# Optimization experiments

Hardware: AMD Instinct MI355X
Metric: run time of the kernel (lower is better)

Reference implementation:

```python
import jax, jax.numpy as jnp
import numpy as np

B, N, E = 2, 2048, 1024
H, D = 16, 64


def setup_inputs() -> dict:
    key = jax.random.key(0)
    k1, k2, k3 = jax.random.split(key, 3)
    x = jax.random.normal(k1, (B, N, E), dtype=jnp.float32)
    Wqkv = jax.random.normal(k2, (3 * H * D, E), dtype=jnp.float32) * 0.02
    bqkv = jnp.zeros((3 * H * D,), dtype=jnp.float32)
    Wout = jax.random.normal(k3, (E, H * D), dtype=jnp.float32) * 0.02
    bout = jnp.zeros((E,), dtype=jnp.float32)
    return {"x": x, "Wqkv": Wqkv, "bqkv": bqkv, "Wout": Wout, "bout": bout}


def reference(x, Wqkv, bqkv, Wout, bout):
    b, n, _ = x.shape
    scale = D ** (-0.5)
    # qkv projection: [b, n, 3*h*d], interpreted as (h, d, qkv) per einops pattern
    qkv = (x @ Wqkv.T + bqkv).reshape(b, n, H, D, 3)
    q = jnp.transpose(qkv[..., 0], (0, 2, 1, 3))  # [b, h, n, d]
    k = jnp.transpose(qkv[..., 1], (0, 2, 1, 3))
    v = jnp.transpose(qkv[..., 2], (0, 2, 1, 3))
    att = jnp.einsum('bhid,bhjd->bhij', q, k) * scale  # [b, h, n, n]
    causal = jnp.tril(jnp.ones((n, n), dtype=bool))
    att = jnp.where(causal, att, -jnp.inf)
    att = jax.nn.softmax(att, axis=-1)
    out = jnp.einsum('bhij,bhjd->bhid', att, v)  # [b, h, n, d]
    out = jnp.transpose(out, (0, 2, 1, 3)).reshape(b, n, H * D)
    return out @ Wout.T + bout
```

## Files before the change

### kernel.cpp

```cpp
#include <hip/hip_runtime.h>
#include <hip/hip_bf16.h>

#define B_ 2
#define N_ 2048
#define E_ 1024
#define H_ 16
#define D_ 64
#define M_ 4096
#define HD_ 1024
#define NT_ 3072

using f32x4  = __attribute__((ext_vector_type(4))) float;
using f32x16 = __attribute__((ext_vector_type(16))) float;
using bf16x8 = __attribute__((ext_vector_type(8))) short;

static __device__ __forceinline__ unsigned short f2bf(float f) {
  union { float f; unsigned u; } v; v.f = f;
  unsigned r = v.u + 0x7FFF + ((v.u >> 16) & 1);
  return (unsigned short)(r >> 16);
}
static __device__ __forceinline__ float bf2f(short s) {
  union { unsigned u; float f; } v; v.u = ((unsigned)(unsigned short)s) << 16; return v.f;
}

static __device__ __forceinline__ void gld16(const void* g, void* l) {
  __builtin_amdgcn_global_load_lds(
      (const __attribute__((address_space(1))) unsigned int*)g,
      (__attribute__((address_space(3))) unsigned int*)l, 16, 0, 0);
}

static __device__ __forceinline__ unsigned cvtpk(float lo, float hi) {
  unsigned r;
  asm("v_cvt_pk_bf16_f32 %0, %1, %2" : "=v"(r) : "v"(lo), "v"(hi));
  return r;
}
static __device__ __forceinline__ void pl32swap(unsigned& a, unsigned& b) {
  asm("v_permlane32_swap_b32 %0, %1" : "+v"(a), "+v"(b));
}


__global__ void k_cvt_x(const float* __restrict__ x, unsigned short* __restrict__ xb) {
  int t = blockIdx.x * 256 + threadIdx.x;
  float4 v = reinterpret_cast<const float4*>(x)[t];
  ushort4 o;
  o.x = f2bf(v.x); o.y = f2bf(v.y); o.z = f2bf(v.z); o.w = f2bf(v.w);
  reinterpret_cast<ushort4*>(xb)[t] = o;
}

__global__ void k_cvt_wqkv(const float* __restrict__ w, const float* __restrict__ bsrc,
                           unsigned short* __restrict__ wb, float* __restrict__ br) {
  int t = blockIdx.x * 256 + threadIdx.x;
  int r = t >> 8;
  int c = (t & 255) * 4;
  int kind = r >> 10, hd = r & 1023;
  int h = hd >> 6, d = hd & 63;
  int rin = h * 192 + d * 3 + kind;
  float s = (kind == 0) ? 0.125f * 1.4426950408889634f : 1.0f;
  float4 v = *reinterpret_cast<const float4*>(w + (size_t)rin * E_ + c);
  ushort4 o;
  o.x = f2bf(v.x * s); o.y = f2bf(v.y * s); o.z = f2bf(v.z * s); o.w = f2bf(v.w * s);
  *reinterpret_cast<ushort4*>(wb + (size_t)r * E_ + c) = o;
  if (c == 0) br[r] = bsrc[rin] * s;
}

__global__ void k_cvt_wout(const float* __restrict__ w, unsigned short* __restrict__ wb) {
  int t = blockIdx.x * 256 + threadIdx.x;
  int r = t >> 8;
  int c = (t & 255) * 4;
  float4 v = *reinterpret_cast<const float4*>(w + (size_t)r * HD_ + c);
  ushort4 o;
  o.x = f2bf(v.x); o.y = f2bf(v.y); o.z = f2bf(v.z); o.w = f2bf(v.w);
  *reinterpret_cast<ushort4*>(wb + (size_t)r * HD_ + c) = o;
}

template <int EPI>
__global__ __launch_bounds__(256, 2) void k_gemm(
    const unsigned short* __restrict__ A,
    const unsigned short* __restrict__ W,
    const float* __restrict__ bias,
    unsigned short* __restrict__ Qo, unsigned short* __restrict__ Ko,
    unsigned short* __restrict__ Vo, float* __restrict__ Fo,
    int M, int Nt, int K)
{
  __shared__ unsigned short As[128 * 32];
  __shared__ unsigned short Bs[128 * 32];
  const int t = threadIdx.x;
  const int w = t >> 6, l = t & 63, lg = l >> 4, lr = l & 15;
  const int wm = w >> 1, wn = w & 1;
  const int row0 = blockIdx.x * 128, col0 = blockIdx.y * 128;

  f32x4 acc[4][4] = {};

  for (int k0 = 0; k0 < K; k0 += 32) {
#pragma unroll
    for (int c = 0; c < 2; ++c) {
      int ci = w * 2 + c;
      int eo = ci * 512 + l * 8;
      int rr = eo >> 5, kk = eo & 31;
      gld16(A + (size_t)(row0 + rr) * K + k0 + kk, (unsigned short*)As + ci * 512);
      gld16(W + (size_t)(col0 + rr) * K + k0 + kk, (unsigned short*)Bs + ci * 512);
    }
    __syncthreads();
    bf16x8 af[4], bf[4];
#pragma unroll
    for (int m = 0; m < 4; ++m)
      af[m] = *reinterpret_cast<const bf16x8*>(&As[(wm * 64 + m * 16 + lr) * 32 + lg * 8]);
#pragma unroll
    for (int n = 0; n < 4; ++n)
      bf[n] = *reinterpret_cast<const bf16x8*>(&Bs[(wn * 64 + n * 16 + lr) * 32 + lg * 8]);
#pragma unroll
    for (int m = 0; m < 4; ++m)
#pragma unroll
      for (int n = 0; n < 4; ++n)
        acc[m][n] = __builtin_amdgcn_mfma_f32_16x16x32_bf16(af[m], bf[n], acc[m][n], 0, 0, 0);
    __syncthreads();
  }

#pragma unroll
  for (int m = 0; m < 4; ++m) {
#pragma unroll
    for (int n = 0; n < 4; ++n) {
      int col = col0 + wn * 64 + n * 16 + lr;
      float bb = bias[col];
#pragma unroll
      for (int rr = 0; rr < 4; ++rr) {
        int ro = row0 + wm * 64 + m * 16 + lg * 4 + rr;
        float val = acc[m][n][rr] + bb;
        if (EPI == 0) {
          int kind = col >> 10, hd = col & 1023, h = hd >> 6, d = hd & 63;
          int bi = ro >> 11, ni = ro & 2047;
          unsigned short bv = f2bf(val);
          size_t bh = (size_t)(bi * H_ + h);
          if (kind == 0)      Qo[(bh * N_ + ni) * D_ + d] = bv;
          else if (kind == 1) Ko[(bh * N_ + ni) * D_ + d] = bv;
          else                Vo[bh * (size_t)(D_ * N_) + (size_t)d * N_ + ni] = bv;
        } else {
          Fo[(size_t)ro * HD_ + col] = val;
        }
      }
    }
  }
}

__global__ __launch_bounds__(256, 3) void k_attn(
    const unsigned short* __restrict__ Q,
    const unsigned short* __restrict__ Kg,
    const unsigned short* __restrict__ Vg,
    unsigned short* __restrict__ O,
    unsigned short* __restrict__ Pp,
    float* __restrict__ Pml)
{
  static const int u_qt[24] = {15,15,14,13,12,11,10, 9,   8, 7,14, 6,13, 5,12, 4,   8, 0, 9, 1,10, 2,11, 3};
  static const int u_t0[24] = { 0,16, 0, 0, 0, 0, 0, 0,   0, 0,16, 0,16, 0,16, 0,  16, 0,16, 0,16, 0,16, 0};
  static const int u_ps[24] = {14,15,12,10, 8, 6, 4, 2,   0,-1,13,-1,11,-1, 9,-1,   1,-1, 3,-1, 5,-1, 7,-1};

  __shared__ unsigned short Ks[2][64 * 64];
  __shared__ unsigned short Vs[2][64 * 64];

  const int t = threadIdx.x;
  const int w = t >> 6, l = t & 63;
  const int lq = l & 31;
  const int hi = l >> 5;
  const int bh = blockIdx.x & 31;
  const int u  = blockIdx.x >> 5;
  const int qt = u_qt[u], t0 = u_t0[u], ps = u_ps[u];
  const int q0 = qt * 128;
  const int r0w = q0 + w * 32;
  const int rtop = r0w + 31;
  const bool splitc0 = (ps >= 0) && (t0 == 0);
  const int tendW = splitc0 ? 16 : ((rtop >> 6) + 1);
  const int tendB = splitc0 ? 16 : (((q0 + 127) >> 6) + 1);

  const unsigned short* Qb = Q  + (size_t)bh * (N_ * D_);
  const unsigned short* Kb = Kg + (size_t)bh * (N_ * D_);
  const unsigned short* Vb = Vg + (size_t)bh * (N_ * D_);

  const int pr  = l >> 3;
  const int pswz = ((l & 7) ^ pr) * 8;
  const unsigned short* KsrcB = Kb + pr * D_ + pswz;
  const unsigned short* VsrcB = Vb + pr * N_ + pswz;

  bf16x8 qf[4];
#pragma unroll
  for (int ks = 0; ks < 4; ++ks)
    qf[ks] = *reinterpret_cast<const bf16x8*>(
        Qb + (size_t)(r0w + lq) * D_ + ks * 16 + hi * 8);

  f32x16 oacc[2] = {};
  float lrun = 0.f;

  {
    const int kv0 = t0 * 64;
#pragma unroll
    for (int c = 0; c < 2; ++c) {
      int cb = w * 2 + c;
      gld16(KsrcB + kv0 * D_ + cb * 512, (unsigned short*)&Ks[0][0] + cb * 512);
      gld16(VsrcB + kv0 + cb * 8 * N_,   (unsigned short*)&Vs[0][0] + cb * 512);
    }
  }
  __syncthreads();
  int buf = 0;

  for (int kt = t0; kt < tendB; ++kt) {
    const int kv0 = kt * 64;

    if (kt + 1 < tendB) {
      const int kv1 = kv0 + 64;
#pragma unroll
      for (int c = 0; c < 2; ++c) {
        int cb = w * 2 + c;
        gld16(KsrcB + kv1 * D_ + cb * 512, (unsigned short*)&Ks[buf ^ 1][0] + cb * 512);
        gld16(VsrcB + kv1 + cb * 8 * N_,   (unsigned short*)&Vs[buf ^ 1][0] + cb * 512);
      }
    }

    if (kt < tendW) {
      bf16x8 kf[2][4], vf[2][4];
#pragma unroll
      for (int ct = 0; ct < 2; ++ct)
#pragma unroll
        for (int ks = 0; ks < 4; ++ks) {
          int row = ct * 32 + lq;
          kf[ct][ks] = *reinterpret_cast<const bf16x8*>(
              &Ks[buf][row * 64 + (((ks * 2 + hi) ^ (lq & 7)) * 8)]);
        }
#pragma unroll
      for (int dt = 0; dt < 2; ++dt)
#pragma unroll
        for (int j = 0; j < 4; ++j) {
          int row = dt * 32 + lq;
          vf[dt][j] = *reinterpret_cast<const bf16x8*>(
              &Vs[buf][row * 64 + (((j * 2 + hi) ^ (lq & 7)) * 8)]);
        }

      f32x16 sct[2];
      __builtin_amdgcn_s_setprio(1);
#pragma unroll
      for (int ct = 0; ct < 2; ++ct) {
        f32x16 z = {};
#pragma unroll
        for (int ks = 0; ks < 4; ++ks)
          z = __builtin_amdgcn_mfma_f32_32x32x16_bf16(kf[ct][ks], qf[ks], z, 0, 0, 0);
        sct[ct] = z;
      }
      __builtin_amdgcn_s_setprio(0);

      if (kv0 + 63 > r0w) {
        int qrow = r0w + lq;
#pragma unroll
        for (int ct = 0; ct < 2; ++ct)
#pragma unroll
          for (int r = 0; r < 16; ++r) {
            int kv = kv0 + ct * 32 + (r & 3) + 8 * (r >> 2) + 4 * hi;
            if (kv > qrow) sct[ct][r] = -1e30f;
          }
      }

      float s16[16];
#pragma unroll
      for (int r = 0; r < 16; ++r) {
        float p0 = exp2f(sct[0][r]);
        float p1 = exp2f(sct[1][r]);
        sct[0][r] = p0; sct[1][r] = p1;
        s16[r] = p0 + p1;
      }
#pragma unroll
      for (int st = 8; st >= 1; st >>= 1)
#pragma unroll
        for (int r = 0; r < 8; ++r)
          if (r < st) s16[r] += s16[r + st];
      lrun += s16[0] + __shfl_xor(s16[0], 32);

      bf16x8 paf[4];
#pragma unroll
      for (int ct = 0; ct < 2; ++ct) {
        unsigned u0 = cvtpk(sct[ct][0],  sct[ct][1]);
        unsigned u1 = cvtpk(sct[ct][2],  sct[ct][3]);
        unsigned u2 = cvtpk(sct[ct][4],  sct[ct][5]);
        unsigned u3 = cvtpk(sct[ct][6],  sct[ct][7]);
        unsigned u4 = cvtpk(sct[ct][8],  sct[ct][9]);
        unsigned u5 = cvtpk(sct[ct][10], sct[ct][11]);
        unsigned u6 = cvtpk(sct[ct][12], sct[ct][13]);
        unsigned u7 = cvtpk(sct[ct][14], sct[ct][15]);
        pl32swap(u0, u2); pl32swap(u1, u3);
        pl32swap(u4, u6); pl32swap(u5, u7);
        union { unsigned uu[4]; bf16x8 v; } c0, c1;
        c0.uu[0] = u0; c0.uu[1] = u1; c0.uu[2] = u2; c0.uu[3] = u3;
        c1.uu[0] = u4; c1.uu[1] = u5; c1.uu[2] = u6; c1.uu[3] = u7;
        paf[ct * 2]     = c0.v;
        paf[ct * 2 + 1] = c1.v;
      }

      __builtin_amdgcn_s_setprio(1);
#pragma unroll
      for (int dt = 0; dt < 2; ++dt)
#pragma unroll
        for (int j = 0; j < 4; ++j)
          oacc[dt] = __builtin_amdgcn_mfma_f32_32x32x16_bf16(paf[j], vf[dt][j], oacc[dt], 0, 0, 0);
      __builtin_amdgcn_s_setprio(0);
    }

    __syncthreads();
    buf ^= 1;
  }

  int bi = bh >> 4, h = bh & 15;
  if (ps < 0) {
    float inv = 1.0f / lrun;
    float iv[16];
#pragma unroll
    for (int r = 0; r < 16; ++r)
      iv[r] = __shfl(inv, (r & 3) + 8 * (r >> 2) + 4 * hi);
#pragma unroll
    for (int dt = 0; dt < 2; ++dt)
#pragma unroll
      for (int r = 0; r < 16; ++r) {
        int qr = r0w + (r & 3) + 8 * (r >> 2) + 4 * hi;
        int d = dt * 32 + lq;
        O[((size_t)(bi * N_ + qr) * H_ + h) * D_ + d] = f2bf(oacc[dt][r] * iv[r]);
      }
  } else {
    unsigned short* pb = Pp + (size_t)(bh * 16 + ps) * (128 * 64);
    float* mb = Pml + (size_t)(bh * 16 + ps) * 128;
#pragma unroll
    for (int dt = 0; dt < 2; ++dt)
#pragma unroll
      for (int r = 0; r < 16; ++r) {
        int rloc = w * 32 + (r & 3) + 8 * (r >> 2) + 4 * hi;
        pb[rloc * 64 + dt * 32 + lq] = f2bf(oacc[dt][r]);
      }
    if (l < 32) {
      int rloc = w * 32 + l;
      mb[rloc] = lrun;
    }
  }
}

__global__ void k_merge(const unsigned short* __restrict__ Pp,
                        const float* __restrict__ Pml,
                        unsigned short* __restrict__ O) {
  int t = blockIdx.x * 256 + threadIdx.x;
  int dseg = t & 7;
  int rloc = (t >> 3) & 127;
  int qt8 = (t >> 10) & 7;
  int bh  = t >> 13;
  size_t b0 = (size_t)(bh * 16 + qt8 * 2) * 128 + rloc;
  size_t b1 = b0 + 128;
  bf16x8 o0 = *reinterpret_cast<const bf16x8*>(Pp + b0 * 64 + dseg * 8);
  bf16x8 o1 = *reinterpret_cast<const bf16x8*>(Pp + b1 * 64 + dseg * 8);
  float l0 = Pml[b0], l1 = Pml[b1];
  float inv = 1.0f / (l0 + l1);
  int n = (qt8 + 8) * 128 + rloc;
  int bi = bh >> 4, h = bh & 15;
  unsigned short* op = O + ((size_t)(bi * N_ + n) * H_ + h) * D_ + dseg * 8;
  bf16x8 res;
#pragma unroll
  for (int j = 0; j < 8; ++j)
    res[j] = (short)f2bf((bf2f(o0[j]) + bf2f(o1[j])) * inv);
  *reinterpret_cast<bf16x8*>(op) = res;
}


extern "C" void kernel_launch(void* const* d_in, const int* in_sizes, int n_in,
                              void* d_out, int out_size, void* d_ws, size_t ws_size,
                              hipStream_t stream) {
  const float* x    = (const float*)d_in[0];
  const float* Wqkv = (const float*)d_in[1];
  const float* bqkv = (const float*)d_in[2];
  const float* Wout = (const float*)d_in[3];
  const float* bout = (const float*)d_in[4];
  float* out = (float*)d_out;

  char* ws = (char*)d_ws;
  unsigned short* xb  = (unsigned short*)ws; ws += (size_t)M_ * E_ * 2;
  unsigned short* wqb = (unsigned short*)ws; ws += (size_t)NT_ * E_ * 2;
  float*          bqr = (float*)ws;          ws += 16384;
  unsigned short* wob = (unsigned short*)ws; ws += (size_t)E_ * HD_ * 2;
  unsigned short* Qb  = (unsigned short*)ws; ws += (size_t)M_ * D_ * H_ * 2;
  unsigned short* Kb  = (unsigned short*)ws; ws += (size_t)M_ * D_ * H_ * 2;
  unsigned short* Vb  = (unsigned short*)ws; ws += (size_t)M_ * D_ * H_ * 2;
  unsigned short* ao  = (unsigned short*)ws; ws += (size_t)M_ * HD_ * 2;

  unsigned short* Pp  = xb;
  float*          Pml = (float*)wqb;

  k_cvt_x<<<(M_ * E_) / 4 / 256, 256, 0, stream>>>(x, xb);
  k_cvt_wqkv<<<NT_, 256, 0, stream>>>(Wqkv, bqkv, wqb, bqr);
  k_cvt_wout<<<E_, 256, 0, stream>>>(Wout, wob);

  k_gemm<0><<<dim3(M_ / 128, NT_ / 128), 256, 0, stream>>>(
      xb, wqb, bqr, Qb, Kb, Vb, nullptr, M_, NT_, E_);

  k_attn<<<768, 256, 0, stream>>>(Qb, Kb, Vb, ao, Pp, Pml);
  k_merge<<<1024, 256, 0, stream>>>(Pp, Pml, ao);

  k_gemm<1><<<dim3(M_ / 128, HD_ / 128), 256, 0, stream>>>(
      ao, wob, bout, nullptr, nullptr, nullptr, out, M_, HD_, E_);
}
```

Measured before the change: 119.0 us.

## Triple-buffer GEMM and attention loads with vmcnt waits, swizzled LDS, smaller out-proj tile

Both the GEMM and attention kernels move from a double-buffered __syncthreads loop to a three-stage ring of global_load_lds prefetches. Each stage is gated by an explicit s_waitcnt vmcnt count and a raw s_barrier, so two tiles are in flight while the current one is consumed. The GEMM LDS tiles gain an XOR swizzle to reduce bank conflicts on fragment reads. The output projection switches to a 64-row tile to double its block count. LDS use rises, which may reduce occupancy, and the hand-coded vmcnt counts must match the exact number of loads issued per stage.

```diff
diff --git a/kernel.cpp b/kernel.cpp
--- a/kernel.cpp
+++ b/kernel.cpp
@@ -36,6 +36,10 @@
 }
 static __device__ __forceinline__ void pl32swap(unsigned& a, unsigned& b) {
   asm("v_permlane32_swap_b32 %0, %1" : "+v"(a), "+v"(b));
+}
+
+static __device__ __forceinline__ int gswz(int row) {
+  return ((row >> 1) & 3) ^ ((row >> 3) & 1);
 }
 
 
@@ -73,7 +77,7 @@
   *reinterpret_cast<ushort4*>(wb + (size_t)r * HD_ + c) = o;
 }
 
-template <int EPI>
+template <int EPI, int BM>
 __global__ __launch_bounds__(256, 2) void k_gemm(
     const unsigned short* __restrict__ A,
     const unsigned short* __restrict__ W,
@@ -82,49 +86,90 @@
     unsigned short* __restrict__ Vo, float* __restrict__ Fo,
     int M, int Nt, int K)
 {
-  __shared__ unsigned short As[128 * 32];
-  __shared__ unsigned short Bs[128 * 32];
+  constexpr int APT = (BM == 128) ? 2 : 1;
+  constexpr int LPI = APT + 2;
+  constexpr int NF  = (BM == 128) ? 4 : 2;
+  __shared__ unsigned short As[3][BM * 32];
+  __shared__ unsigned short Bs[3][128 * 32];
   const int t = threadIdx.x;
   const int w = t >> 6, l = t & 63, lg = l >> 4, lr = l & 15;
-  const int wm = w >> 1, wn = w & 1;
-  const int row0 = blockIdx.x * 128, col0 = blockIdx.y * 128;
-
-  f32x4 acc[4][4] = {};
-
-  for (int k0 = 0; k0 < K; k0 += 32) {
+  const int wrow0 = (BM == 128) ? (w >> 1) * 64 : 0;
+  const int wcol0 = (BM == 128) ? (w & 1) * 64 : w * 32;
+  const int row0 = blockIdx.x * BM, col0 = blockIdx.y * 128;
+  const int NT = K >> 5;
+
+  f32x4 acc[4][NF] = {};
+
+  auto stage = [&](int b, int k0) {
+#pragma unroll
+    for (int c = 0; c < APT; ++c) {
+      int ci = w * APT + c;
+      int row = ci * 16 + (l >> 2);
+      int sub = (l & 3) ^ gswz(row);
+      gld16(A + (size_t)(row0 + row) * K + k0 + sub * 8,
+            (unsigned short*)&As[b][0] + ci * 512);
+    }
 #pragma unroll
     for (int c = 0; c < 2; ++c) {
       int ci = w * 2 + c;
-      int eo = ci * 512 + l * 8;
-      int rr = eo >> 5, kk = eo & 31;
-      gld16(A + (size_t)(row0 + rr) * K + k0 + kk, (unsigned short*)As + ci * 512);
-      gld16(W + (size_t)(col0 + rr) * K + k0 + kk, (unsigned short*)Bs + ci * 512);
-    }
-    __syncthreads();
-    bf16x8 af[4], bf[4];
+      int row = ci * 16 + (l >> 2);
+      int sub = (l & 3) ^ gswz(row);
+      gld16(W + (size_t)(col0 + row) * K + k0 + sub * 8,
+            (unsigned short*)&Bs[b][0] + ci * 512);
+    }
+  };
+
+  stage(0, 0);
+  stage(1, 32);
+
+  for (int kt = 0; kt < NT; ++kt) {
+    const int ib = kt % 3;
+    if (kt + 2 < NT) stage((kt + 2) % 3, (kt + 2) * 32);
+    const int na = NT - 1 - kt;
+    if (na >= 2) {
+      if constexpr (LPI == 4) asm volatile("s_waitcnt vmcnt(8)" ::: "memory");
+      else                    asm volatile("s_waitcnt vmcnt(6)" ::: "memory");
+    } else if (na == 1) {
+      if constexpr (LPI == 4) asm volatile("s_waitcnt vmcnt(4)" ::: "memory");
+      else                    asm volatile("s_waitcnt vmcnt(3)" ::: "memory");
+    } else {
+      asm volatile("s_waitcnt vmcnt(0)" ::: "memory");
+    }
+    asm volatile("s_barrier" ::: "memory");
+
+    bf16x8 af[4], bf[NF];
+#pragma unroll
+    for (int m = 0; m < 4; ++m) {
+      int row = wrow0 + m * 16 + lr;
+      af[m] = *reinterpret_cast<const bf16x8*>(
+          &As[ib][row * 32 + ((lg ^ gswz(row)) * 8)]);
+    }
+#pragma unroll
+    for (int n = 0; n < NF; ++n) {
+      int row = wcol0 + n * 16 + lr;
+      bf[n] = *reinterpret_cast<const bf16x8*>(
+          &Bs[ib][row * 32 + ((lg ^ gswz(row)) * 8)]);
+    }
+    __builtin_amdgcn_s_setprio(1);
 #pragma unroll
     for (int m = 0; m < 4; ++m)
-      af[m] = *reinterpret_cast<const bf16x8*>(&As[(wm * 64 + m * 16 + lr) * 32 + lg * 8]);
-#pragma unroll
-    for (int n = 0; n < 4; ++n)
-      bf[n] = *reinterpret_cast<const bf16x8*>(&Bs[(wn * 64 + n * 16 + lr) * 32 + lg * 8]);
-#pragma unroll
-    for (int m = 0; m < 4; ++m)
-#pragma unroll
-      for (int n = 0; n < 4; ++n)
+#pragma unroll
+      for (int n = 0; n < NF; ++n)
         acc[m][n] = __builtin_amdgcn_mfma_f32_16x16x32_bf16(af[m], bf[n], acc[m][n], 0, 0, 0);
-    __syncthreads();
+    __builtin_amdgcn_s_setprio(0);
+
+    asm volatile("s_barrier" ::: "memory");
   }
 
 #pragma unroll
   for (int m = 0; m < 4; ++m) {
 #pragma unroll
-    for (int n = 0; n < 4; ++n) {
-      int col = col0 + wn * 64 + n * 16 + lr;
+    for (int n = 0; n < NF; ++n) {
+      int col = col0 + wcol0 + n * 16 + lr;
       float bb = bias[col];
 #pragma unroll
       for (int rr = 0; rr < 4; ++rr) {
-        int ro = row0 + wm * 64 + m * 16 + lg * 4 + rr;
+        int ro = row0 + wrow0 + m * 16 + lg * 4 + rr;
         float val = acc[m][n][rr] + bb;
         if (EPI == 0) {
           int kind = col >> 10, hd = col & 1023, h = hd >> 6, d = hd & 63;
@@ -154,8 +199,8 @@
   static const int u_t0[24] = { 0,16, 0, 0, 0, 0, 0, 0,   0, 0,16, 0,16, 0,16, 0,  16, 0,16, 0,16, 0,16, 0};
   static const int u_ps[24] = {14,15,12,10, 8, 6, 4, 2,   0,-1,13,-1,11,-1, 9,-1,   1,-1, 3,-1, 5,-1, 7,-1};
 
-  __shared__ unsigned short Ks[2][64 * 64];
-  __shared__ unsigned short Vs[2][64 * 64];
+  __shared__ unsigned short Ks[3][64 * 64];
+  __shared__ unsigned short Vs[3][64 * 64];
 
   const int t = threadIdx.x;
   const int w = t >> 6, l = t & 63;
@@ -189,32 +234,30 @@
   f32x16 oacc[2] = {};
   float lrun = 0.f;
 
-  {
-    const int kv0 = t0 * 64;
+  auto stage = [&](int b, int kt_) {
+    const int kv = kt_ * 64;
 #pragma unroll
     for (int c = 0; c < 2; ++c) {
       int cb = w * 2 + c;
-      gld16(KsrcB + kv0 * D_ + cb * 512, (unsigned short*)&Ks[0][0] + cb * 512);
-      gld16(VsrcB + kv0 + cb * 8 * N_,   (unsigned short*)&Vs[0][0] + cb * 512);
-    }
-  }
-  __syncthreads();
-  int buf = 0;
+      gld16(KsrcB + kv * D_ + cb * 512, (unsigned short*)&Ks[b][0] + cb * 512);
+      gld16(VsrcB + kv + cb * 8 * N_,   (unsigned short*)&Vs[b][0] + cb * 512);
+    }
+  };
+
+  stage(0, t0);
+  if (t0 + 1 < tendB) stage(1, t0 + 1);
 
   for (int kt = t0; kt < tendB; ++kt) {
-    const int kv0 = kt * 64;
-
-    if (kt + 1 < tendB) {
-      const int kv1 = kv0 + 64;
-#pragma unroll
-      for (int c = 0; c < 2; ++c) {
-        int cb = w * 2 + c;
-        gld16(KsrcB + kv1 * D_ + cb * 512, (unsigned short*)&Ks[buf ^ 1][0] + cb * 512);
-        gld16(VsrcB + kv1 + cb * 8 * N_,   (unsigned short*)&Vs[buf ^ 1][0] + cb * 512);
-      }
-    }
+    const int ib = (kt - t0) % 3;
+    if (kt + 2 < tendB) stage((kt - t0 + 2) % 3, kt + 2);
+    const int na = tendB - 1 - kt;
+    if (na >= 2)      asm volatile("s_waitcnt vmcnt(8)" ::: "memory");
+    else if (na == 1) asm volatile("s_waitcnt vmcnt(4)" ::: "memory");
+    else              asm volatile("s_waitcnt vmcnt(0)" ::: "memory");
+    asm volatile("s_barrier" ::: "memory");
 
     if (kt < tendW) {
+      const int kv0 = kt * 64;
       bf16x8 kf[2][4], vf[2][4];
 #pragma unroll
       for (int ct = 0; ct < 2; ++ct)
@@ -222,7 +265,7 @@
         for (int ks = 0; ks < 4; ++ks) {
           int row = ct * 32 + lq;
           kf[ct][ks] = *reinterpret_cast<const bf16x8*>(
-              &Ks[buf][row * 64 + (((ks * 2 + hi) ^ (lq & 7)) * 8)]);
+              &Ks[ib][row * 64 + (((ks * 2 + hi) ^ (lq & 7)) * 8)]);
         }
 #pragma unroll
       for (int dt = 0; dt < 2; ++dt)
@@ -230,7 +273,7 @@
         for (int j = 0; j < 4; ++j) {
           int row = dt * 32 + lq;
           vf[dt][j] = *reinterpret_cast<const bf16x8*>(
-              &Vs[buf][row * 64 + (((j * 2 + hi) ^ (lq & 7)) * 8)]);
+              &Vs[ib][row * 64 + (((j * 2 + hi) ^ (lq & 7)) * 8)]);
         }
 
       f32x16 sct[2];
@@ -300,8 +343,7 @@
       __builtin_amdgcn_s_setprio(0);
     }
 
-    __syncthreads();
-    buf ^= 1;
+    asm volatile("s_barrier" ::: "memory");
   }
 
   int bi = bh >> 4, h = bh & 15;
@@ -388,12 +430,12 @@
   k_cvt_wqkv<<<NT_, 256, 0, stream>>>(Wqkv, bqkv, wqb, bqr);
   k_cvt_wout<<<E_, 256, 0, stream>>>(Wout, wob);
 
-  k_gemm<0><<<dim3(M_ / 128, NT_ / 128), 256, 0, stream>>>(
+  k_gemm<0, 128><<<dim3(M_ / 128, NT_ / 128), 256, 0, stream>>>(
       xb, wqb, bqr, Qb, Kb, Vb, nullptr, M_, NT_, E_);
 
   k_attn<<<768, 256, 0, stream>>>(Qb, Kb, Vb, ao, Pp, Pml);
   k_merge<<<1024, 256, 0, stream>>>(Pp, Pml, ao);
 
-  k_gemm<1><<<dim3(M_ / 128, HD_ / 128), 256, 0, stream>>>(
+  k_gemm<1, 64><<<dim3(M_ / 64, HD_ / 128), 256, 0, stream>>>(
       ao, wob, bout, nullptr, nullptr, nullptr, out, M_, HD_, E_);
 }
```

After: 118.5 us. About the same (-0.4%).
